# Kernel optimization log

Measured on AMD Instinct MI355X. Metric: run time of the kernel, lower is better.

The kernel has to match this reference:

```python
import jax, jax.numpy as jnp
import numpy as np

B, S, E, H = 4, 2048, 1024, 16
D = E // H  # head_dim = 64


def setup_inputs() -> dict:
    key = jax.random.key(0)
    k1, k2, k3, k4, k5 = jax.random.split(key, 5)
    # xavier_uniform bounds
    lim_qkv = float(np.sqrt(6.0 / (E + 3 * E)))
    lim_out = float(np.sqrt(6.0 / (E + E)))
    return {
        "inp": jax.random.normal(k1, (B, S, E), dtype=jnp.float32),
        "qkv_w": jax.random.uniform(k2, (3 * E, E), minval=-lim_qkv, maxval=lim_qkv, dtype=jnp.float32),
        "qkv_b": jnp.zeros((3 * E,), dtype=jnp.float32),
        "out_w": jax.random.uniform(k3, (E, E), minval=-lim_out, maxval=lim_out, dtype=jnp.float32),
        "out_b": jnp.zeros((E,), dtype=jnp.float32),
    }


def reference(inp, qkv_w, qkv_b, out_w, out_b):
    b, s, _ = inp.shape
    # qkv projection: [b,s,3E]
    qkv = jnp.einsum("bse,fe->bsf", inp, qkv_w) + qkv_b
    qkv = qkv.reshape(b, s, 3, H, D).transpose(2, 0, 3, 1, 4)  # [3,b,h,s,d]
    q, k, v = qkv[0], qkv[1], qkv[2]
    scale = 1.0 / jnp.sqrt(jnp.float32(D))
    scores = jnp.einsum("bhqd,bhkd->bhqk", q, k) * scale
    attn = jax.nn.softmax(scores, axis=-1)  # dropout = identity (eval mode)
    ctx = jnp.einsum("bhqk,bhkd->bhqd", attn, v)
    ctx = ctx.transpose(0, 2, 1, 3).reshape(b, s, E)
    out = jnp.einsum("bse,fe->bsf", ctx, out_w) + out_b
    return out
```

## Files before the change

### kernel.cpp

```cpp
#include <hip/hip_runtime.h>
#include <stdint.h>

typedef unsigned short u16;
typedef __bf16 bf16x8 __attribute__((ext_vector_type(8)));
typedef float f32x4 __attribute__((ext_vector_type(4)));
typedef float f32x16 __attribute__((ext_vector_type(16)));

#define DEV static __device__ __forceinline__

DEV u16 f2bf(float f) {
  uint32_t u = __float_as_uint(f);
  u += 0x7fffu + ((u >> 16) & 1u);
  return (u16)(u >> 16);
}

DEV void g2l16(const void* g, void* l) {
  __builtin_amdgcn_global_load_lds(
      (__attribute__((address_space(1))) void*)(g),
      (__attribute__((address_space(3))) void*)(l), 16, 0, 0);
}

DEV f32x4 mfma16(bf16x8 a, bf16x8 b, f32x4 c) {
  return __builtin_amdgcn_mfma_f32_16x16x32_bf16(a, b, c, 0, 0, 0);
}
DEV f32x16 mfma32(bf16x8 a, bf16x8 b, f32x16 c) {
  return __builtin_amdgcn_mfma_f32_32x32x16_bf16(a, b, c, 0, 0, 0);
}

DEV bf16x8 lds_ld(const char* p) { return *(const bf16x8*)p; }

DEV float fexp2(float x) {
  float r;
  asm("v_exp_f32 %0, %1" : "=v"(r) : "v"(x));
  return r;
}

DEV uint32_t cvtpk(float lo, float hi) {
  uint32_t r;
  asm("v_cvt_pk_bf16_f32 %0, %1, %2" : "=v"(r) : "v"(lo), "v"(hi));
  return r;
}
DEV void pswap(uint32_t& a, uint32_t& b) {
  auto r = __builtin_amdgcn_permlane32_swap((int)a, (int)b, false, false);
  a = (uint32_t)r[0];
  b = (uint32_t)r[1];
}
DEV float xhalf_sum(float x) {
  auto r = __builtin_amdgcn_permlane32_swap(__float_as_int(x), __float_as_int(x), false, false);
  return __int_as_float(r[0]) + __int_as_float(r[1]);
}

__global__ __launch_bounds__(256) void cvt_kernel(const float* __restrict__ in,
                                                  u16* __restrict__ out, int n4) {
  int i = blockIdx.x * 256 + threadIdx.x;
  if (i >= n4) return;
  float4 v = ((const float4*)in)[i];
  ushort4 o;
  o.x = f2bf(v.x); o.y = f2bf(v.y); o.z = f2bf(v.z); o.w = f2bf(v.w);
  ((ushort4*)out)[i] = o;
}

template<int EPI>
__global__ __launch_bounds__(512, 2) void gemm256(
    const u16* __restrict__ A, const u16* __restrict__ B,
    const float* __restrict__ bias, void* __restrict__ C,
    u16* __restrict__ vT,
    int M, int N, int K, int qcols, float qscale, int vcol0) {
  __shared__ char sm[147456];
  const int tid = threadIdx.x;
  const int w = tid >> 6, l = tid & 63;
  const int wm = w >> 1, wn = w & 1;
  const int bm0 = blockIdx.x * 256, bn0 = blockIdx.y * 128;
  const int lr = l >> 3, lsl = (l & 7) ^ lr;
  const u16* gA = A + (size_t)(bm0 + w * 8 + lr) * K + lsl * 8;
  const u16* gB = B + (size_t)(bn0 + w * 8 + lr) * K + lsl * 8;

  auto stage = [&](int t) {
    char* base = sm + (t % 3) * 49152 + w * 1024;
    const u16* a = gA + t * 64;
    const u16* b = gB + t * 64;
#pragma unroll
    for (int r = 0; r < 4; ++r)
      g2l16(a + (size_t)(r * 64) * K, base + r * 8192);
#pragma unroll
    for (int r = 0; r < 2; ++r)
      g2l16(b + (size_t)(r * 64) * K, base + 32768 + r * 8192);
  };

  f32x4 acc[4][4] = {};
  const int NT = K / 64;
  stage(0); stage(1);
  asm volatile("s_waitcnt vmcnt(6)" ::: "memory");
  __builtin_amdgcn_s_barrier();
  __builtin_amdgcn_sched_barrier(0);
  for (int t = 0; t < NT; ++t) {
    if (t + 2 < NT) stage(t + 2);
    const char* bufA = sm + (t % 3) * 49152;
    const char* bufB = bufA + 32768;
#pragma unroll
    for (int ks = 0; ks < 2; ++ks) {
      bf16x8 af[4], bfr[4];
#pragma unroll
      for (int i = 0; i < 4; ++i) {
        const int rowA = wm * 64 + i * 16 + (l & 15);
        af[i] = lds_ld(bufA + rowA * 128 +
                       ((ks * 64 + ((l >> 4) << 4)) ^ ((rowA & 7) << 4)));
      }
#pragma unroll
      for (int j = 0; j < 4; ++j) {
        const int rowB = wn * 64 + j * 16 + (l & 15);
        bfr[j] = lds_ld(bufB + rowB * 128 +
                        ((ks * 64 + ((l >> 4) << 4)) ^ ((rowB & 7) << 4)));
      }
#pragma unroll
      for (int i = 0; i < 4; ++i)
#pragma unroll
        for (int j = 0; j < 4; ++j)
          acc[i][j] = mfma16(af[i], bfr[j], acc[i][j]);
    }
    if (t + 2 < NT) {
      asm volatile("s_waitcnt vmcnt(6)" ::: "memory");
    } else if (t + 1 < NT) {
      asm volatile("s_waitcnt vmcnt(0)" ::: "memory");
    }
    if (t + 1 < NT) {
      __builtin_amdgcn_s_barrier();
      __builtin_amdgcn_sched_barrier(0);
    }
  }
  const int cr = (l >> 4) * 4, cc = l & 15;
  if (EPI == 1 && bn0 >= vcol0) {
#pragma unroll
    for (int i = 0; i < 4; ++i) {
      const int gr = bm0 + wm * 64 + i * 16 + cr;
      const int b = gr >> 11, s = gr & 2047;
#pragma unroll
      for (int j = 0; j < 4; ++j) {
        const int gc = bn0 + wn * 64 + j * 16 + cc;
        const float bv = bias[gc];
        const int vc = gc - vcol0;
        u16* dst = vT + ((size_t)((b * 16 + (vc >> 6)) * 64 + (vc & 63))) * 2048 + s;
        ushort4 pk;
        pk.x = f2bf(acc[i][j][0] + bv);
        pk.y = f2bf(acc[i][j][1] + bv);
        pk.z = f2bf(acc[i][j][2] + bv);
        pk.w = f2bf(acc[i][j][3] + bv);
        *(ushort4*)dst = pk;
      }
    }
    return;
  }
#pragma unroll
  for (int i = 0; i < 4; ++i) {
    const int gr = bm0 + wm * 64 + i * 16 + cr;
#pragma unroll
    for (int j = 0; j < 4; ++j) {
      const int gc = bn0 + wn * 64 + j * 16 + cc;
      const float bv = bias[gc];
      const float scl = (gc < qcols) ? qscale : 1.0f;
#pragma unroll
      for (int r = 0; r < 4; ++r) {
        const float v = (acc[i][j][r] + bv) * scl;
        if (EPI == 0) ((float*)C)[(size_t)(gr + r) * N + gc] = v;
        else          ((u16*)C)[(size_t)(gr + r) * N + gc] = f2bf(v);
      }
    }
  }
}

__global__ __launch_bounds__(256, 2) void attn(const u16* __restrict__ qkv,
                                               const u16* __restrict__ vT,
                                               u16* __restrict__ ctx) {
  constexpr int S = 2048, E = 1024, TE = 3072, NT = S / 64;
  const int id = blockIdx.x;
  const int x = id & 7, j = id >> 3;
  const int bh = x * 8 + (j & 7), qt = j >> 3;
  const int b = bh >> 4, h = bh & 15;
  const int tid = threadIdx.x, w = tid >> 6, l = tid & 63;
  const int q = l & 31, hi = l >> 5;
  __shared__ char sm[2][16384];

  const int qglobA = qt * 256 + w * 64 + q;
  const int qglobB = qglobA + 32;
  const u16* qpA = qkv + (size_t)(b * S + qglobA) * TE + h * 64 + hi * 8;
  const u16* qpB = qkv + (size_t)(b * S + qglobB) * TE + h * 64 + hi * 8;
  bf16x8 qfA[4], qfB[4];
#pragma unroll
  for (int d = 0; d < 4; ++d) {
    qfA[d] = *(const bf16x8*)(qpA + d * 16);
    qfB[d] = *(const bf16x8*)(qpB + d * 16);
  }

  const int lr = l >> 3, lsl = (l & 7) ^ lr;
  const u16* gK = qkv + (size_t)(b * S) * TE + E + h * 64 + lsl * 8;
  const u16* gV = vT + (size_t)(bh * 64) * S + lsl * 8;

  auto stage = [&](int t, int pp) {
    char* bk = sm[pp] + w * 2048;
#pragma unroll
    for (int i = 0; i < 2; ++i) {
      const int row = w * 16 + i * 8 + lr;
      g2l16(gK + (size_t)(t * 64 + row) * TE, bk + i * 1024);
      g2l16(gV + (size_t)row * S + t * 64, bk + 8192 + i * 1024);
    }
  };

  f32x16 o0A = {}, o1A = {}, o0B = {}, o1B = {};
  float lsumA = 0.f, lsumB = 0.f;

  auto expsum = [&](f32x16& e, float& ls) {
    float ts[4] = {0.f, 0.f, 0.f, 0.f};
#pragma unroll
    for (int r = 0; r < 16; ++r) {
      e[r] = fexp2(e[r]);
      ts[r & 3] += e[r];
    }
    ls += (ts[0] + ts[1]) + (ts[2] + ts[3]);
  };
  auto mkfrag = [&](const f32x16& e, bf16x8& P0, bf16x8& P1) {
    uint32_t a0 = cvtpk(e[0], e[1]), c0 = cvtpk(e[4], e[5]);
    uint32_t a1 = cvtpk(e[2], e[3]), c1 = cvtpk(e[6], e[7]);
    pswap(a0, c0); pswap(a1, c1);
    uint32_t a2 = cvtpk(e[8], e[9]), c2 = cvtpk(e[12], e[13]);
    uint32_t a3 = cvtpk(e[10], e[11]), c3 = cvtpk(e[14], e[15]);
    pswap(a2, c2); pswap(a3, c3);
    union { uint32_t u[4]; bf16x8 v; } t0, t1;
    t0.u[0] = a0; t0.u[1] = a1; t0.u[2] = c0; t0.u[3] = c1;
    t1.u[0] = a2; t1.u[1] = a3; t1.u[2] = c2; t1.u[3] = c3;
    P0 = t0.v; P1 = t1.v;
  };

  int pp = 0;
  stage(0, 0);
  __syncthreads();
  for (int t = 0; t < NT; ++t) {
    if (t + 1 < NT) stage(t + 1, pp ^ 1);
    const char* bK = sm[pp];
    const char* bV = sm[pp] + 8192;
    const int swz = (q & 7) << 4;
#pragma unroll
    for (int s = 0; s < 2; ++s) {
      const char* kr = bK + (s * 32 + q) * 128;
      bf16x8 kf[4];
#pragma unroll
      for (int d = 0; d < 4; ++d) kf[d] = lds_ld(kr + (((d * 2 + hi) << 4) ^ swz));
      f32x16 stA = {}, stB = {};
      __builtin_amdgcn_s_setprio(1);
#pragma unroll
      for (int d = 0; d < 4; ++d) {
        stA = mfma32(kf[d], qfA[d], stA);
        stB = mfma32(kf[d], qfB[d], stB);
      }
      __builtin_amdgcn_s_setprio(0);
      const int s0 = (((s * 4 + hi) << 4) ^ swz);
      const int s1 = (((s * 4 + 2 + hi) << 4) ^ swz);
      const bf16x8 va0 = lds_ld(bV + q * 128 + s0);
      const bf16x8 va1 = lds_ld(bV + q * 128 + s1);
      const bf16x8 vb0 = lds_ld(bV + (32 + q) * 128 + s0);
      const bf16x8 vb1 = lds_ld(bV + (32 + q) * 128 + s1);
      expsum(stA, lsumA);
      expsum(stB, lsumB);
      bf16x8 pA0, pA1, pB0, pB1;
      mkfrag(stA, pA0, pA1);
      mkfrag(stB, pB0, pB1);
      __builtin_amdgcn_s_setprio(1);
      o0A = mfma32(va0, pA0, o0A); o0B = mfma32(va0, pB0, o0B);
      o0A = mfma32(va1, pA1, o0A); o0B = mfma32(va1, pB1, o0B);
      o1A = mfma32(vb0, pA0, o1A); o1B = mfma32(vb0, pB0, o1B);
      o1A = mfma32(vb1, pA1, o1A); o1B = mfma32(vb1, pB1, o1B);
      __builtin_amdgcn_s_setprio(0);
    }
    __syncthreads();
    pp ^= 1;
  }
  auto writeo = [&](const f32x16& e0, const f32x16& e1, float ls, int qg) {
    const float inv = 1.0f / xhalf_sum(ls);
    u16* cp = ctx + (size_t)(b * S + qg) * E + h * 64 + 4 * hi;
#pragma unroll
    for (int g = 0; g < 4; ++g) {
      ushort4 pk0, pk1;
      pk0.x = f2bf(e0[4 * g + 0] * inv); pk0.y = f2bf(e0[4 * g + 1] * inv);
      pk0.z = f2bf(e0[4 * g + 2] * inv); pk0.w = f2bf(e0[4 * g + 3] * inv);
      *(ushort4*)(cp + 8 * g) = pk0;
      pk1.x = f2bf(e1[4 * g + 0] * inv); pk1.y = f2bf(e1[4 * g + 1] * inv);
      pk1.z = f2bf(e1[4 * g + 2] * inv); pk1.w = f2bf(e1[4 * g + 3] * inv);
      *(ushort4*)(cp + 32 + 8 * g) = pk1;
    }
  };
  writeo(o0A, o1A, lsumA, qglobA);
  writeo(o0B, o1B, lsumB, qglobB);
}

extern "C" void kernel_launch(void* const* d_in, const int* in_sizes, int n_in,
                              void* d_out, int out_size, void* d_ws, size_t ws_size,
                              hipStream_t stream) {
  (void)in_sizes; (void)n_in; (void)out_size;
  const float* inp   = (const float*)d_in[0];
  const float* qkv_w = (const float*)d_in[1];
  const float* qkv_b = (const float*)d_in[2];
  const float* out_w = (const float*)d_in[3];
  const float* out_b = (const float*)d_in[4];
  char* ws = (char*)d_ws;
  if (ws_size < 92274688u) return;

  u16* inp_b  = (u16*)(ws);
  u16* qkvw_b = (u16*)(ws + 16777216);
  u16* outw_b = (u16*)(ws + 23068672);
  u16* qkvo   = (u16*)(ws + 25165824);
  u16* vTb    = (u16*)(ws + 75497472);
  u16* ctx    = inp_b;

  const float cexp = 0.18033688f;

  hipLaunchKernelGGL(cvt_kernel, dim3(8192), dim3(256), 0, stream, inp, inp_b, 2097152);
  hipLaunchKernelGGL(cvt_kernel, dim3(3072), dim3(256), 0, stream, qkv_w, qkvw_b, 786432);
  hipLaunchKernelGGL(cvt_kernel, dim3(1024), dim3(256), 0, stream, out_w, outw_b, 262144);
  hipLaunchKernelGGL((gemm256<1>), dim3(32, 24), dim3(512), 0, stream,
                     inp_b, qkvw_b, qkv_b, (void*)qkvo, vTb,
                     8192, 3072, 1024, 1024, cexp, 2048);
  hipLaunchKernelGGL(attn, dim3(512), dim3(256), 0, stream, qkvo, vTb, ctx);
  hipLaunchKernelGGL((gemm256<0>), dim3(32, 8), dim3(512), 0, stream,
                     ctx, outw_b, out_b, d_out, (u16*)nullptr,
                     8192, 1024, 1024, 0, 1.0f, 1 << 30);
}
```

Measured before the change: 176.7 us.

## Restructure GEMM into double-buffered ping-pong schedule with interleaved loads

Rewrites the 256x128 bf16 GEMM main loop from a three-stage ring buffer into a two-buffer schedule. Each K tile is split into two half-phases, and global-to-LDS loads for later tiles are interleaved between them. Warp layout changes from 4x2 to 2x4, so each wave owns 128x32 of output. MFMA blocks are bracketed with s_setprio and extra barriers so that loads and math from different waves overlap. LDS use drops from 144KB to 96KB, at the cost of more barriers per tile and trickier vmcnt bookkeeping.

```diff
diff --git a/kernel.cpp b/kernel.cpp
--- a/kernel.cpp
+++ b/kernel.cpp
@@ -34,7 +34,6 @@
   asm("v_exp_f32 %0, %1" : "=v"(r) : "v"(x));
   return r;
 }
-
 DEV uint32_t cvtpk(float lo, float hi) {
   uint32_t r;
   asm("v_cvt_pk_bf16_f32 %0, %1, %2" : "=v"(r) : "v"(lo), "v"(hi));
@@ -48,6 +47,10 @@
 DEV float xhalf_sum(float x) {
   auto r = __builtin_amdgcn_permlane32_swap(__float_as_int(x), __float_as_int(x), false, false);
   return __int_as_float(r[0]) + __int_as_float(r[1]);
+}
+DEV void vwait(int n) {
+  if (n == 2) asm volatile("s_waitcnt vmcnt(2)" ::: "memory");
+  else if (n == 0) asm volatile("s_waitcnt vmcnt(0)" ::: "memory");
 }
 
 __global__ __launch_bounds__(256) void cvt_kernel(const float* __restrict__ in,
@@ -66,101 +69,141 @@
     const float* __restrict__ bias, void* __restrict__ C,
     u16* __restrict__ vT,
     int M, int N, int K, int qcols, float qscale, int vcol0) {
-  __shared__ char sm[147456];
+  __shared__ char sm[98304];
   const int tid = threadIdx.x;
   const int w = tid >> 6, l = tid & 63;
-  const int wm = w >> 1, wn = w & 1;
+  const int wm = w >> 2, wn = w & 3;
   const int bm0 = blockIdx.x * 256, bn0 = blockIdx.y * 128;
   const int lr = l >> 3, lsl = (l & 7) ^ lr;
   const u16* gA = A + (size_t)(bm0 + w * 8 + lr) * K + lsl * 8;
   const u16* gB = B + (size_t)(bn0 + w * 8 + lr) * K + lsl * 8;
-
-  auto stage = [&](int t) {
-    char* base = sm + (t % 3) * 49152 + w * 1024;
-    const u16* a = gA + t * 64;
-    const u16* b = gB + t * 64;
-#pragma unroll
-    for (int r = 0; r < 4; ++r)
-      g2l16(a + (size_t)(r * 64) * K, base + r * 8192);
-#pragma unroll
-    for (int r = 0; r < 2; ++r)
-      g2l16(b + (size_t)(r * 64) * K, base + 32768 + r * 8192);
-  };
-
-  f32x4 acc[4][4] = {};
-  const int NT = K / 64;
-  stage(0); stage(1);
-  asm volatile("s_waitcnt vmcnt(6)" ::: "memory");
+  const int NT = K / 64, NU = NT / 2;
+  const int la = l & 15, hs = l >> 4;
+
+  auto stA = [&](int t, int qa) {
+    g2l16(gA + ((size_t)(qa * 64) * K + t * 64),
+          sm + (t & 1) * 32768 + (qa * 64 + w * 8) * 128);
+  };
+  auto stB = [&](int t, int hb) {
+    g2l16(gB + ((size_t)(hb * 64) * K + t * 64),
+          sm + 65536 + (t & 1) * 16384 + (hb * 64 + w * 8) * 128);
+  };
+
+  f32x4 acc[8][2] = {};
+
+  auto tileC = [&](int buf, auto&& s1, auto&& s2, int ev1, int ev2) {
+    const char* bA = sm + buf * 32768;
+    const char* bB = sm + 65536 + buf * 16384;
+    bf16x8 af[4][2], bfr[2][2];
+#pragma unroll
+    for (int m = 0; m < 4; ++m) {
+      const int row = wm * 128 + m * 16 + la;
+      const int sw = (row & 7) << 4;
+#pragma unroll
+      for (int ks = 0; ks < 2; ++ks)
+        af[m][ks] = lds_ld(bA + row * 128 + (((ks * 4 + hs) << 4) ^ sw));
+    }
+#pragma unroll
+    for (int nf = 0; nf < 2; ++nf) {
+      const int row = wn * 32 + nf * 16 + la;
+      const int sw = (row & 7) << 4;
+#pragma unroll
+      for (int ks = 0; ks < 2; ++ks)
+        bfr[nf][ks] = lds_ld(bB + row * 128 + (((ks * 4 + hs) << 4) ^ sw));
+    }
+    s1();
+    __builtin_amdgcn_s_barrier();
+    asm volatile("s_waitcnt lgkmcnt(0)" ::: "memory");
+    __builtin_amdgcn_sched_barrier(0);
+    __builtin_amdgcn_s_setprio(1);
+#pragma unroll
+    for (int m = 0; m < 4; ++m)
+#pragma unroll
+      for (int nf = 0; nf < 2; ++nf)
+#pragma unroll
+        for (int ks = 0; ks < 2; ++ks)
+          acc[m][nf] = mfma16(af[m][ks], bfr[nf][ks], acc[m][nf]);
+    __builtin_amdgcn_s_setprio(0);
+    vwait(ev1);
+    __builtin_amdgcn_s_barrier();
+    __builtin_amdgcn_sched_barrier(0);
+#pragma unroll
+    for (int m = 0; m < 4; ++m) {
+      const int row = wm * 128 + 64 + m * 16 + la;
+      const int sw = (row & 7) << 4;
+#pragma unroll
+      for (int ks = 0; ks < 2; ++ks)
+        af[m][ks] = lds_ld(bA + row * 128 + (((ks * 4 + hs) << 4) ^ sw));
+    }
+    s2();
+    __builtin_amdgcn_s_barrier();
+    asm volatile("s_waitcnt lgkmcnt(0)" ::: "memory");
+    __builtin_amdgcn_sched_barrier(0);
+    __builtin_amdgcn_s_setprio(1);
+#pragma unroll
+    for (int m = 0; m < 4; ++m)
+#pragma unroll
+      for (int nf = 0; nf < 2; ++nf)
+#pragma unroll
+        for (int ks = 0; ks < 2; ++ks)
+          acc[4 + m][nf] = mfma16(af[m][ks], bfr[nf][ks], acc[4 + m][nf]);
+    __builtin_amdgcn_s_setprio(0);
+    vwait(ev2);
+    __builtin_amdgcn_s_barrier();
+    __builtin_amdgcn_sched_barrier(0);
+  };
+
+  stA(0, 0); stA(0, 1); stA(0, 2); stA(0, 3); stB(0, 0); stB(0, 1);
+  stA(1, 0); stA(1, 2);
+  asm volatile("s_waitcnt vmcnt(2)" ::: "memory");
   __builtin_amdgcn_s_barrier();
   __builtin_amdgcn_sched_barrier(0);
-  for (int t = 0; t < NT; ++t) {
-    if (t + 2 < NT) stage(t + 2);
-    const char* bufA = sm + (t % 3) * 49152;
-    const char* bufB = bufA + 32768;
-#pragma unroll
-    for (int ks = 0; ks < 2; ++ks) {
-      bf16x8 af[4], bfr[4];
-#pragma unroll
-      for (int i = 0; i < 4; ++i) {
-        const int rowA = wm * 64 + i * 16 + (l & 15);
-        af[i] = lds_ld(bufA + rowA * 128 +
-                       ((ks * 64 + ((l >> 4) << 4)) ^ ((rowA & 7) << 4)));
-      }
-#pragma unroll
-      for (int j = 0; j < 4; ++j) {
-        const int rowB = wn * 64 + j * 16 + (l & 15);
-        bfr[j] = lds_ld(bufB + rowB * 128 +
-                        ((ks * 64 + ((l >> 4) << 4)) ^ ((rowB & 7) << 4)));
-      }
-#pragma unroll
-      for (int i = 0; i < 4; ++i)
-#pragma unroll
-        for (int j = 0; j < 4; ++j)
-          acc[i][j] = mfma16(af[i], bfr[j], acc[i][j]);
-    }
-    if (t + 2 < NT) {
-      asm volatile("s_waitcnt vmcnt(6)" ::: "memory");
-    } else if (t + 1 < NT) {
-      asm volatile("s_waitcnt vmcnt(0)" ::: "memory");
-    }
-    if (t + 1 < NT) {
-      __builtin_amdgcn_s_barrier();
-      __builtin_amdgcn_sched_barrier(0);
-    }
-  }
-  const int cr = (l >> 4) * 4, cc = l & 15;
+
+  for (int u = 0; u < NU; ++u) {
+    const int t1 = 2 * u + 1, t2 = 2 * u + 2, t3 = 2 * u + 3;
+    tileC(0,
+          [&] { stA(t1, 1); stA(t1, 3); stB(t1, 0); },
+          [&] { stB(t1, 1); if (t2 < NT) { stA(t2, 0); stA(t2, 2); } },
+          -1, (t2 < NT) ? 2 : 0);
+    tileC(1,
+          [&] { if (t2 < NT) { stA(t2, 1); stA(t2, 3); stB(t2, 0); } },
+          [&] { if (t2 < NT) stB(t2, 1); if (t3 < NT) { stA(t3, 0); stA(t3, 2); } },
+          -1, (t3 < NT) ? 2 : ((t2 < NT) ? 0 : -1));
+  }
+
+  const int cr = hs * 4, cc = la;
   if (EPI == 1 && bn0 >= vcol0) {
 #pragma unroll
-    for (int i = 0; i < 4; ++i) {
-      const int gr = bm0 + wm * 64 + i * 16 + cr;
+    for (int mf = 0; mf < 8; ++mf) {
+      const int gr = bm0 + wm * 128 + (mf >> 2) * 64 + (mf & 3) * 16 + cr;
       const int b = gr >> 11, s = gr & 2047;
 #pragma unroll
-      for (int j = 0; j < 4; ++j) {
-        const int gc = bn0 + wn * 64 + j * 16 + cc;
+      for (int nf = 0; nf < 2; ++nf) {
+        const int gc = bn0 + wn * 32 + nf * 16 + cc;
         const float bv = bias[gc];
         const int vc = gc - vcol0;
         u16* dst = vT + ((size_t)((b * 16 + (vc >> 6)) * 64 + (vc & 63))) * 2048 + s;
         ushort4 pk;
-        pk.x = f2bf(acc[i][j][0] + bv);
-        pk.y = f2bf(acc[i][j][1] + bv);
-        pk.z = f2bf(acc[i][j][2] + bv);
-        pk.w = f2bf(acc[i][j][3] + bv);
+        pk.x = f2bf(acc[mf][nf][0] + bv);
+        pk.y = f2bf(acc[mf][nf][1] + bv);
+        pk.z = f2bf(acc[mf][nf][2] + bv);
+        pk.w = f2bf(acc[mf][nf][3] + bv);
         *(ushort4*)dst = pk;
       }
     }
     return;
   }
 #pragma unroll
-  for (int i = 0; i < 4; ++i) {
-    const int gr = bm0 + wm * 64 + i * 16 + cr;
-#pragma unroll
-    for (int j = 0; j < 4; ++j) {
-      const int gc = bn0 + wn * 64 + j * 16 + cc;
+  for (int mf = 0; mf < 8; ++mf) {
+    const int gr = bm0 + wm * 128 + (mf >> 2) * 64 + (mf & 3) * 16 + cr;
+#pragma unroll
+    for (int nf = 0; nf < 2; ++nf) {
+      const int gc = bn0 + wn * 32 + nf * 16 + cc;
       const float bv = bias[gc];
       const float scl = (gc < qcols) ? qscale : 1.0f;
 #pragma unroll
       for (int r = 0; r < 4; ++r) {
-        const float v = (acc[i][j][r] + bv) * scl;
+        const float v = (acc[mf][nf][r] + bv) * scl;
         if (EPI == 0) ((float*)C)[(size_t)(gr + r) * N + gc] = v;
         else          ((u16*)C)[(size_t)(gr + r) * N + gc] = f2bf(v);
       }
```

Result: no change. 177.4 us (+0.4%).
